# Performance work log

Measured on AMD Instinct MI355X. Metric: run time of the kernel, lower is better.

Reference implementation:

```python
import jax, jax.numpy as jnp
import numpy as np

EPS = 1e-12          # sinkhorn_knopp epsilon
LOW, HIGH = 0.02, 0.98  # SquashedSigmoid bounds
N_ITERS = 10         # num_iterations
BATCH = 2097152


def setup_inputs() -> dict:
    key = jax.random.key(0)
    ks = jax.random.split(key, 9)
    dims = [6, 64, 32, 16, 9]
    inp = {"margins": jax.random.uniform(ks[0], (BATCH, 6), jnp.float32, 0.05, 1.0)}
    for i in range(4):
        fi, fo = dims[i], dims[i + 1]
        inp[f"W{i+1}"] = jax.random.normal(ks[1 + 2 * i], (fi, fo), jnp.float32) / np.float32(np.sqrt(fi))
        inp[f"b{i+1}"] = jnp.zeros((fo,), jnp.float32)
    return inp


def _mlp(x, W1, b1, W2, b2, W3, b3, W4, b4):
    h = jax.nn.relu(x @ W1 + b1)
    h = jax.nn.relu(h @ W2 + b2)
    h = jax.nn.relu(h @ W3 + b3)
    return h @ W4 + b4  # [B, 9]


def _tau(p4):
    # user-supplied tau: 4 positive params -> 3x3 matrix; 2x2 block padded with ones
    B = p4.shape[0]
    A = jnp.ones((B, 3, 3), p4.dtype)
    return A.at[:, :2, :2].set(p4.reshape(B, 2, 2))


def _sinkhorn_knopp(A, r, c):
    # batched row/col balancing; per-sample A is 3x3, r/c are length-3 margins
    for _ in range(N_ITERS):
        A = A * (r[:, :, None] / (A.sum(axis=2, keepdims=True) + EPS))
        A = A * (c[:, None, :] / (A.sum(axis=1, keepdims=True) + EPS))
    return A


def reference(margins, W1, b1, W2, b2, W3, b3, W4, b4):
    B = margins.shape[0]
    M, F = margins[:, 0:3], margins[:, 3:6]
    pars = _mlp(margins, W1, b1, W2, b2, W3, b3, W4, b4)
    muc = _tau(jnp.exp(pars[:, 0:4]))                     # [B,3,3]
    sqs = lambda x: LOW + (HIGH - LOW) * jax.nn.sigmoid(x)
    shm, shf = sqs(pars[:, 4:6]), sqs(pars[:, 6:8])
    V = jnp.exp(pars[:, -1])                              # [B]
    ones = jnp.ones((B, 1), margins.dtype)
    shm0 = jnp.concatenate([shm, ones], axis=1)           # [B,3]
    shf0 = jnp.concatenate([shf, ones], axis=1)
    mucm0, muc0f = M * shm0, F * shf0                     # row / col margins
    mum0, mu0f = M * (1 - shm0), F * (1 - shf0)
    muc = _sinkhorn_knopp(muc, mucm0, muc0f)              # [B,3,3]
    top = jnp.concatenate([muc, mum0[:, :, None]], axis=2)                    # [B,3,4]
    bot = jnp.concatenate([mu0f[:, None, :], jnp.zeros((B, 1, 1), margins.dtype)], axis=2)  # [B,1,4]
    mus = jnp.concatenate([top, bot], axis=1)             # [B,4,4]
    return (mus, V)
```

## Files before the change

kernel.cpp:

```cpp
#include <hip/hip_runtime.h>

typedef _Float16 f16x8 __attribute__((ext_vector_type(8)));
typedef _Float16 f16x4 __attribute__((ext_vector_type(4)));
typedef __fp16   fp16x2 __attribute__((ext_vector_type(2)));
typedef float    f32x4 __attribute__((ext_vector_type(4)));

static constexpr float kLOW  = 0.02f;
static constexpr float kHIGH = 0.98f;

__device__ __forceinline__ float fast_rcp(float v) {
    return __builtin_amdgcn_rcpf(v);
}
__device__ __forceinline__ float fast_sigmoid(float v) {
    return fast_rcp(1.0f + __expf(-v));
}
__device__ __forceinline__ unsigned int relu_pk(float a, float b) {
    fp16x2 r = __builtin_amdgcn_cvt_pkrtz(fmaxf(a, 0.0f), fmaxf(b, 0.0f));
    return __builtin_bit_cast(unsigned int, r);
}

enum : int {
    WS_A1 = 0,
    WS_A2 = 4096,
    WS_A3 = 8192,
    WS_A4 = 9216,
    WS_B1 = 10240,
    WS_B2 = 14336,
    WS_B3 = 16384,
    WS_B4 = 17408,
    WS_TOTAL = 18432
};

__global__ __launch_bounds__(256) void prep_frags(
    const float* __restrict__ W1, const float* __restrict__ b1,
    const float* __restrict__ W2, const float* __restrict__ b2,
    const float* __restrict__ W3, const float* __restrict__ b3,
    const float* __restrict__ W4, const float* __restrict__ b4,
    char* __restrict__ ws)
{
    const int lane = threadIdx.x & 63;
    const int wid  = threadIdx.x >> 6;
    const int n16  = lane & 15;
    const int q    = lane >> 4;

    if (wid == 0) {
#pragma unroll
        for (int mt = 0; mt < 4; ++mt) {
            f16x8 a;
#pragma unroll
            for (int j = 0; j < 8; ++j) a[j] = (_Float16)0.0f;
            if (q == 0) {
#pragma unroll
                for (int j = 0; j < 6; ++j)
                    a[j] = (_Float16)W1[j * 64 + mt * 16 + n16];
            }
            ((f16x8*)(ws + WS_A1))[mt * 64 + lane] = a;
        }
#pragma unroll
        for (int mt = 0; mt < 4; ++mt)
            ((f32x4*)(ws + WS_B1))[mt * 64 + lane] = *(const f32x4*)(b1 + mt * 16 + q * 4);
    } else if (wid == 1) {
#pragma unroll
        for (int mt = 0; mt < 2; ++mt)
#pragma unroll
            for (int kt = 0; kt < 2; ++kt) {
                f16x8 a;
#pragma unroll
                for (int j = 0; j < 8; ++j)
                    a[j] = (_Float16)W2[(kt * 32 + q * 8 + j) * 32 + mt * 16 + n16];
                ((f16x8*)(ws + WS_A2))[(mt * 2 + kt) * 64 + lane] = a;
            }
    } else if (wid == 2) {
        f16x8 a3;
#pragma unroll
        for (int j = 0; j < 8; ++j)
            a3[j] = (_Float16)W3[(q * 8 + j) * 16 + n16];
        ((f16x8*)(ws + WS_A3))[lane] = a3;
        f16x8 a4;
#pragma unroll
        for (int j = 0; j < 8; ++j) {
            const int k = q * 8 + j;
            a4[j] = (k < 16 && n16 < 9) ? (_Float16)W4[k * 9 + n16] : (_Float16)0.0f;
        }
        ((f16x8*)(ws + WS_A4))[lane] = a4;
    } else {
#pragma unroll
        for (int mt = 0; mt < 2; ++mt)
            ((f32x4*)(ws + WS_B2))[mt * 64 + lane] = *(const f32x4*)(b2 + mt * 16 + q * 4);
        ((f32x4*)(ws + WS_B3))[lane] = *(const f32x4*)(b3 + q * 4);
        f32x4 bb;
#pragma unroll
        for (int r = 0; r < 4; ++r) {
            const int m = q * 4 + r;
            bb[r] = (m < 9) ? b4[m] : 0.0f;
        }
        ((f32x4*)(ws + WS_B4))[lane] = bb;
    }
}

__global__ __launch_bounds__(256, 4) void sinkhorn_mlp_mfma(
    const float* __restrict__ margins, const char* __restrict__ ws,
    float* __restrict__ out_mus, float* __restrict__ out_V, int B)
{
    __shared__ __align__(16) char smem_all[4 * 8192];
    const int lane = threadIdx.x & 63;
    const int wid  = threadIdx.x >> 6;
    char* smem = smem_all + wid * 8192;

    const int n16 = lane & 15;
    const int q   = lane >> 4;

    const int wbase = blockIdx.x * 256 + wid * 64;
    const int row   = wbase + lane;
    const int rowC  = row < B ? row : (B - 1);

    float x[6];
    {
        const float2* mp = (const float2*)(margins + (size_t)rowC * 6);
        const float2 a = mp[0], b = mp[1], c = mp[2];
        x[0] = a.x; x[1] = a.y; x[2] = b.x; x[3] = b.y; x[4] = c.x; x[5] = c.y;
    }

    {
        f16x8 xr;
#pragma unroll
        for (int j = 0; j < 8; ++j) xr[j] = (_Float16)0.0f;
#pragma unroll
        for (int i = 0; i < 6; ++i) xr[i] = (_Float16)x[i];
        *(f16x8*)(smem + 7168 + lane * 16) = xr;
    }

    f16x8 A1[4], A2w[2][2], A3w, A4w;
#pragma unroll
    for (int mt = 0; mt < 4; ++mt) A1[mt] = ((const f16x8*)(ws + WS_A1))[mt * 64 + lane];
#pragma unroll
    for (int mt = 0; mt < 2; ++mt)
#pragma unroll
        for (int kt = 0; kt < 2; ++kt)
            A2w[mt][kt] = ((const f16x8*)(ws + WS_A2))[(mt * 2 + kt) * 64 + lane];
    A3w = ((const f16x8*)(ws + WS_A3))[lane];
    A4w = ((const f16x8*)(ws + WS_A4))[lane];

    f32x4 b1v[4], b2v[2], b3v, b4v;
#pragma unroll
    for (int mt = 0; mt < 4; ++mt) b1v[mt] = ((const f32x4*)(ws + WS_B1))[mt * 64 + lane];
#pragma unroll
    for (int mt = 0; mt < 2; ++mt) b2v[mt] = ((const f32x4*)(ws + WS_B2))[mt * 64 + lane];
    b3v = ((const f32x4*)(ws + WS_B3))[lane];
    b4v = ((const f32x4*)(ws + WS_B4))[lane];

    f16x8 BX[4];
    if (q == 0) {
#pragma unroll
        for (int nt = 0; nt < 4; ++nt)
            BX[nt] = *(const f16x8*)(smem + 7168 + (nt * 16 + n16) * 16);
    } else {
#pragma unroll
        for (int nt = 0; nt < 4; ++nt)
#pragma unroll
            for (int j = 0; j < 8; ++j) BX[nt][j] = (_Float16)0.0f;
    }
#pragma unroll
    for (int mt = 0; mt < 4; ++mt) {
#pragma unroll
        for (int nt = 0; nt < 4; ++nt) {
            f32x4 C = b1v[mt];
            C = __builtin_amdgcn_mfma_f32_16x16x32_f16(A1[mt], BX[nt], C, 0, 0, 0);
            uint2 hv;
            hv.x = relu_pk(C[0], C[1]);
            hv.y = relu_pk(C[2], C[3]);
            const int r = nt * 16 + n16;
            const int col = (mt * 32 + q * 8) ^ ((r & 7) << 4);
            *(uint2*)(smem + r * 128 + col) = hv;
        }
    }

    f16x8 H1f[4][2];
#pragma unroll
    for (int nt = 0; nt < 4; ++nt) {
        const int r = nt * 16 + n16;
#pragma unroll
        for (int kt = 0; kt < 2; ++kt) {
            const int col = (kt * 64 + q * 16) ^ ((r & 7) << 4);
            H1f[nt][kt] = *(const f16x8*)(smem + r * 128 + col);
        }
    }
#pragma unroll
    for (int mt = 0; mt < 2; ++mt) {
#pragma unroll
        for (int nt = 0; nt < 4; ++nt) {
            f32x4 C = b2v[mt];
            C = __builtin_amdgcn_mfma_f32_16x16x32_f16(A2w[mt][0], H1f[nt][0], C, 0, 0, 0);
            C = __builtin_amdgcn_mfma_f32_16x16x32_f16(A2w[mt][1], H1f[nt][1], C, 0, 0, 0);
            uint2 hv;
            hv.x = relu_pk(C[0], C[1]);
            hv.y = relu_pk(C[2], C[3]);
            *(uint2*)(smem + (nt*16 + n16) * 80 + mt*32 + q*8) = hv;
        }
    }

    f16x8 H2f[4];
#pragma unroll
    for (int nt = 0; nt < 4; ++nt)
        H2f[nt] = *(const f16x8*)(smem + (nt*16 + n16) * 80 + q*16);
#pragma unroll
    for (int nt = 0; nt < 4; ++nt) {
        f32x4 C = b3v;
        C = __builtin_amdgcn_mfma_f32_16x16x32_f16(A3w, H2f[nt], C, 0, 0, 0);
        f16x4 hv;
#pragma unroll
        for (int r = 0; r < 4; ++r) hv[r] = (_Float16)fmaxf(C[r], 0.0f);
        *(f16x4*)(smem + (nt*16 + n16) * 32 + q*8) = hv;
    }

    f16x8 B4[4];
    if (q < 2) {
#pragma unroll
        for (int nt = 0; nt < 4; ++nt)
            B4[nt] = *(const f16x8*)(smem + (nt*16 + n16) * 32 + q * 16);
    } else {
#pragma unroll
        for (int nt = 0; nt < 4; ++nt)
#pragma unroll
            for (int j = 0; j < 8; ++j) B4[nt][j] = (_Float16)0.0f;
    }
#pragma unroll
    for (int nt = 0; nt < 4; ++nt) {
        f32x4 C = b4v;
        C = __builtin_amdgcn_mfma_f32_16x16x32_f16(A4w, B4[nt], C, 0, 0, 0);
        *(f32x4*)(smem + 2560 + (nt*16 + n16) * 80 + q * 16) = C;
    }

    float p[9];
    {
        const char* pr = smem + 2560 + lane * 80;
        *(f32x4*)&p[0] = *(const f32x4*)(pr);
        *(f32x4*)&p[4] = *(const f32x4*)(pr + 16);
        p[8] = *(const float*)(pr + 32);
    }

    const float K00 = __expf(p[0]), K01 = __expf(p[1]);
    const float K10 = __expf(p[2]), K11 = __expf(p[3]);

    const float sh_m0 = kLOW + (kHIGH - kLOW) * fast_sigmoid(p[4]);
    const float sh_m1 = kLOW + (kHIGH - kLOW) * fast_sigmoid(p[5]);
    const float sh_f0 = kLOW + (kHIGH - kLOW) * fast_sigmoid(p[6]);
    const float sh_f1 = kLOW + (kHIGH - kLOW) * fast_sigmoid(p[7]);
    const float V = __expf(p[8]);

    const float M0 = x[0], M1 = x[1], M2 = x[2];
    const float F0 = x[3], F1 = x[4], F2 = x[5];

    const float r0 = M0 * sh_m0, r1 = M1 * sh_m1, r2 = M2;
    const float c0 = F0 * sh_f0, c1 = F1 * sh_f1, c2 = F2;
    const float mum0_0 = M0 * (1.0f - sh_m0), mum0_1 = M1 * (1.0f - sh_m1);
    const float mu0f_0 = F0 * (1.0f - sh_f0), mu0f_1 = F1 * (1.0f - sh_f1);

    const float rc2 = fast_rcp(c2);
    const float g0 = c0 * rc2, g1 = c1 * rc2;
    float v0 = 1.0f, v1 = 1.0f;
    float u0, u1, u2;
#pragma unroll
    for (int it = 0; it < 9; ++it) {
        const float s0 = fmaf(K00, v0, fmaf(K01, v1, 1.0f));
        const float s1 = fmaf(K10, v0, fmaf(K11, v1, 1.0f));
        const float s2 = v0 + v1 + 1.0f;
        u0 = r0 * fast_rcp(s0);
        u1 = r1 * fast_rcp(s1);
        u2 = r2 * fast_rcp(s2);
        const float t0 = fmaf(K00, u0, fmaf(K10, u1, u2));
        const float t1 = fmaf(K01, u0, fmaf(K11, u1, u2));
        const float t2 = u0 + u1 + u2;
        v0 = g0 * (t2 * fast_rcp(t0));
        v1 = g1 * (t2 * fast_rcp(t1));
    }
    float vf0, vf1, vf2;
    {
        const float s0 = fmaf(K00, v0, fmaf(K01, v1, 1.0f));
        const float s1 = fmaf(K10, v0, fmaf(K11, v1, 1.0f));
        const float s2 = v0 + v1 + 1.0f;
        u0 = r0 * fast_rcp(s0);
        u1 = r1 * fast_rcp(s1);
        u2 = r2 * fast_rcp(s2);
        const float t0 = fmaf(K00, u0, fmaf(K10, u1, u2));
        const float t1 = fmaf(K01, u0, fmaf(K11, u1, u2));
        const float t2 = u0 + u1 + u2;
        vf0 = c0 * fast_rcp(t0);
        vf1 = c1 * fast_rcp(t1);
        vf2 = c2 * fast_rcp(t2);
    }
    const float A00 = u0 * K00 * vf0, A01 = u0 * K01 * vf1, A02 = u0 * vf2;
    const float A10 = u1 * K10 * vf0, A11 = u1 * K11 * vf1, A12 = u1 * vf2;
    const float A20 = u2 * vf0,       A21 = u2 * vf1,       A22 = u2 * vf2;

    {
        char* ob = smem + 2560;
        f32x4* s = (f32x4*)(ob + lane * 80);
        s[0] = f32x4{A00, A01, A02, mum0_0};
        s[1] = f32x4{A10, A11, A12, mum0_1};
        s[2] = f32x4{A20, A21, A22, 0.0f};
        s[3] = f32x4{mu0f_0, mu0f_1, 0.0f, 0.0f};

        if (wbase + 64 <= B) {
            float* og = out_mus + (size_t)wbase * 16;
#pragma unroll
            for (int k = 0; k < 4; ++k) {
                const int g = k * 64 + lane;
                const int r = g >> 2, c = g & 3;
                f32x4 v = *(const f32x4*)(ob + r * 80 + c * 16);
                *(f32x4*)(og + (size_t)g * 4) = v;
            }
            out_V[wbase + lane] = V;
        } else if (row < B) {
            float* og = out_mus + (size_t)row * 16;
            const char* sr = ob + lane * 80;
#pragma unroll
            for (int c = 0; c < 4; ++c)
                *(f32x4*)(og + c * 4) = *(const f32x4*)(sr + c * 16);
            out_V[row] = V;
        }
    }
}

extern "C" void kernel_launch(void* const* d_in, const int* in_sizes, int n_in,
                              void* d_out, int out_size, void* d_ws, size_t ws_size,
                              hipStream_t stream) {
    const float* margins = (const float*)d_in[0];
    const float* W1 = (const float*)d_in[1];
    const float* b1 = (const float*)d_in[2];
    const float* W2 = (const float*)d_in[3];
    const float* b2 = (const float*)d_in[4];
    const float* W3 = (const float*)d_in[5];
    const float* b3 = (const float*)d_in[6];
    const float* W4 = (const float*)d_in[7];
    const float* b4 = (const float*)d_in[8];

    const int B = in_sizes[0] / 6;
    float* out_mus = (float*)d_out;
    float* out_V   = out_mus + (size_t)B * 16;
    char*  ws      = (char*)d_ws;

    hipLaunchKernelGGL(prep_frags, dim3(1), dim3(256), 0, stream,
                       W1, b1, W2, b2, W3, b3, W4, b4, ws);

    dim3 block(256);
    dim3 grid((B + 255) / 256);
    hipLaunchKernelGGL(sinkhorn_mlp_mfma, grid, block, 0, stream,
                       margins, ws, out_mus, out_V, B);
}
```

Baseline: 214.1 us.

## Process two row groups per thread and pack Sinkhorn math into float2 vectors

Each wave now handles 128 rows in two halves, reusing the weight fragments loaded into registers, and the grid is halved. The Sinkhorn iteration and the elementwise math run on float2 pairs so the compiler can emit packed FP32 instructions and get more independent work per thread. W4 and b4 are pre-scaled by log2(e) so exp becomes a native exp2, removing a multiply per exponential. This raises register pressure, which may lower occupancy, and the store epilogue now runs twice per thread.

```diff
diff --git a/kernel.cpp b/kernel.cpp
--- a/kernel.cpp
+++ b/kernel.cpp
@@ -4,19 +4,40 @@
 typedef _Float16 f16x4 __attribute__((ext_vector_type(4)));
 typedef __fp16   fp16x2 __attribute__((ext_vector_type(2)));
 typedef float    f32x4 __attribute__((ext_vector_type(4)));
+typedef float    f32x2 __attribute__((ext_vector_type(2)));
 
 static constexpr float kLOW  = 0.02f;
 static constexpr float kHIGH = 0.98f;
+static constexpr float kLog2e = 1.44269504088896340736f;
 
 __device__ __forceinline__ float fast_rcp(float v) {
     return __builtin_amdgcn_rcpf(v);
 }
-__device__ __forceinline__ float fast_sigmoid(float v) {
-    return fast_rcp(1.0f + __expf(-v));
+__device__ __forceinline__ float fast_exp2(float v) {
+#if __has_builtin(__builtin_amdgcn_exp2f)
+    return __builtin_amdgcn_exp2f(v);
+#else
+    return exp2f(v);
+#endif
 }
 __device__ __forceinline__ unsigned int relu_pk(float a, float b) {
     fp16x2 r = __builtin_amdgcn_cvt_pkrtz(fmaxf(a, 0.0f), fmaxf(b, 0.0f));
     return __builtin_bit_cast(unsigned int, r);
+}
+
+__device__ __forceinline__ f32x2 fma2(f32x2 a, f32x2 b, f32x2 c) {
+    return f32x2{fmaf(a.x, b.x, c.x), fmaf(a.y, b.y, c.y)};
+}
+__device__ __forceinline__ f32x2 rcp2(f32x2 v) {
+    return f32x2{fast_rcp(v.x), fast_rcp(v.y)};
+}
+__device__ __forceinline__ f32x2 exp2_2(f32x2 v) {
+    return f32x2{fast_exp2(v.x), fast_exp2(v.y)};
+}
+__device__ __forceinline__ f32x2 sqs2(f32x2 v) {
+    f32x2 e = exp2_2(f32x2{-v.x, -v.y});
+    f32x2 s = rcp2(f32x2{1.0f + e.x, 1.0f + e.y});
+    return f32x2{kLOW + (kHIGH - kLOW) * s.x, kLOW + (kHIGH - kLOW) * s.y};
 }
 
 enum : int {
@@ -80,7 +101,8 @@
 #pragma unroll
         for (int j = 0; j < 8; ++j) {
             const int k = q * 8 + j;
-            a4[j] = (k < 16 && n16 < 9) ? (_Float16)W4[k * 9 + n16] : (_Float16)0.0f;
+            a4[j] = (k < 16 && n16 < 9) ? (_Float16)(W4[k * 9 + n16] * kLog2e)
+                                        : (_Float16)0.0f;
         }
         ((f16x8*)(ws + WS_A4))[lane] = a4;
     } else {
@@ -92,7 +114,7 @@
 #pragma unroll
         for (int r = 0; r < 4; ++r) {
             const int m = q * 4 + r;
-            bb[r] = (m < 9) ? b4[m] : 0.0f;
+            bb[r] = (m < 9) ? b4[m] * kLog2e : 0.0f;
         }
         ((f32x4*)(ws + WS_B4))[lane] = bb;
     }
@@ -110,24 +132,17 @@
     const int n16 = lane & 15;
     const int q   = lane >> 4;
 
-    const int wbase = blockIdx.x * 256 + wid * 64;
-    const int row   = wbase + lane;
-    const int rowC  = row < B ? row : (B - 1);
-
-    float x[6];
-    {
+    const int wbase = blockIdx.x * 512 + wid * 128;
+
+    float xx[2][6];
+#pragma unroll
+    for (int h = 0; h < 2; ++h) {
+        const int row  = wbase + h * 64 + lane;
+        const int rowC = row < B ? row : (B - 1);
         const float2* mp = (const float2*)(margins + (size_t)rowC * 6);
         const float2 a = mp[0], b = mp[1], c = mp[2];
-        x[0] = a.x; x[1] = a.y; x[2] = b.x; x[3] = b.y; x[4] = c.x; x[5] = c.y;
-    }
-
-    {
-        f16x8 xr;
-#pragma unroll
-        for (int j = 0; j < 8; ++j) xr[j] = (_Float16)0.0f;
-#pragma unroll
-        for (int i = 0; i < 6; ++i) xr[i] = (_Float16)x[i];
-        *(f16x8*)(smem + 7168 + lane * 16) = xr;
+        xx[h][0] = a.x; xx[h][1] = a.y; xx[h][2] = b.x;
+        xx[h][3] = b.y; xx[h][4] = c.x; xx[h][5] = c.y;
     }
 
     f16x8 A1[4], A2w[2][2], A3w, A4w;
@@ -149,160 +164,179 @@
     b3v = ((const f32x4*)(ws + WS_B3))[lane];
     b4v = ((const f32x4*)(ws + WS_B4))[lane];
 
-    f16x8 BX[4];
-    if (q == 0) {
+    float pp[2][9];
+#pragma unroll
+    for (int h = 0; h < 2; ++h) {
+        {
+            f16x8 xr;
+#pragma unroll
+            for (int j = 0; j < 8; ++j) xr[j] = (_Float16)0.0f;
+#pragma unroll
+            for (int i = 0; i < 6; ++i) xr[i] = (_Float16)xx[h][i];
+            *(f16x8*)(smem + 7168 + lane * 16) = xr;
+        }
+
+        f16x8 BX[4];
+        if (q == 0) {
+#pragma unroll
+            for (int nt = 0; nt < 4; ++nt)
+                BX[nt] = *(const f16x8*)(smem + 7168 + (nt * 16 + n16) * 16);
+        } else {
+#pragma unroll
+            for (int nt = 0; nt < 4; ++nt)
+#pragma unroll
+                for (int j = 0; j < 8; ++j) BX[nt][j] = (_Float16)0.0f;
+        }
+#pragma unroll
+        for (int mt = 0; mt < 4; ++mt) {
+#pragma unroll
+            for (int nt = 0; nt < 4; ++nt) {
+                f32x4 C = b1v[mt];
+                C = __builtin_amdgcn_mfma_f32_16x16x32_f16(A1[mt], BX[nt], C, 0, 0, 0);
+                uint2 hv;
+                hv.x = relu_pk(C[0], C[1]);
+                hv.y = relu_pk(C[2], C[3]);
+                const int r = nt * 16 + n16;
+                const int col = (mt * 32 + q * 8) ^ ((r & 7) << 4);
+                *(uint2*)(smem + r * 128 + col) = hv;
+            }
+        }
+
+        f16x8 H1f[4][2];
+#pragma unroll
+        for (int nt = 0; nt < 4; ++nt) {
+            const int r = nt * 16 + n16;
+#pragma unroll
+            for (int kt = 0; kt < 2; ++kt) {
+                const int col = (kt * 64 + q * 16) ^ ((r & 7) << 4);
+                H1f[nt][kt] = *(const f16x8*)(smem + r * 128 + col);
+            }
+        }
+#pragma unroll
+        for (int mt = 0; mt < 2; ++mt) {
+#pragma unroll
+            for (int nt = 0; nt < 4; ++nt) {
+                f32x4 C = b2v[mt];
+                C = __builtin_amdgcn_mfma_f32_16x16x32_f16(A2w[mt][0], H1f[nt][0], C, 0, 0, 0);
+                C = __builtin_amdgcn_mfma_f32_16x16x32_f16(A2w[mt][1], H1f[nt][1], C, 0, 0, 0);
+                uint2 hv;
+                hv.x = relu_pk(C[0], C[1]);
+                hv.y = relu_pk(C[2], C[3]);
+                *(uint2*)(smem + (nt*16 + n16) * 80 + mt*32 + q*8) = hv;
+            }
+        }
+
+        f16x8 H2f[4];
 #pragma unroll
         for (int nt = 0; nt < 4; ++nt)
-            BX[nt] = *(const f16x8*)(smem + 7168 + (nt * 16 + n16) * 16);
-    } else {
-#pragma unroll
-        for (int nt = 0; nt < 4; ++nt)
-#pragma unroll
-            for (int j = 0; j < 8; ++j) BX[nt][j] = (_Float16)0.0f;
-    }
-#pragma unroll
-    for (int mt = 0; mt < 4; ++mt) {
+            H2f[nt] = *(const f16x8*)(smem + (nt*16 + n16) * 80 + q*16);
 #pragma unroll
         for (int nt = 0; nt < 4; ++nt) {
-            f32x4 C = b1v[mt];
-            C = __builtin_amdgcn_mfma_f32_16x16x32_f16(A1[mt], BX[nt], C, 0, 0, 0);
-            uint2 hv;
-            hv.x = relu_pk(C[0], C[1]);
-            hv.y = relu_pk(C[2], C[3]);
-            const int r = nt * 16 + n16;
-            const int col = (mt * 32 + q * 8) ^ ((r & 7) << 4);
-            *(uint2*)(smem + r * 128 + col) = hv;
-        }
-    }
-
-    f16x8 H1f[4][2];
-#pragma unroll
-    for (int nt = 0; nt < 4; ++nt) {
-        const int r = nt * 16 + n16;
-#pragma unroll
-        for (int kt = 0; kt < 2; ++kt) {
-            const int col = (kt * 64 + q * 16) ^ ((r & 7) << 4);
-            H1f[nt][kt] = *(const f16x8*)(smem + r * 128 + col);
-        }
-    }
-#pragma unroll
-    for (int mt = 0; mt < 2; ++mt) {
+            f32x4 C = b3v;
+            C = __builtin_amdgcn_mfma_f32_16x16x32_f16(A3w, H2f[nt], C, 0, 0, 0);
+            f16x4 hv;
+#pragma unroll
+            for (int r = 0; r < 4; ++r) hv[r] = (_Float16)fmaxf(C[r], 0.0f);
+            *(f16x4*)(smem + (nt*16 + n16) * 32 + q*8) = hv;
+        }
+
+        f16x8 B4[4];
+        if (q < 2) {
+#pragma unroll
+            for (int nt = 0; nt < 4; ++nt)
+                B4[nt] = *(const f16x8*)(smem + (nt*16 + n16) * 32 + q * 16);
+        } else {
+#pragma unroll
+            for (int nt = 0; nt < 4; ++nt)
+#pragma unroll
+                for (int j = 0; j < 8; ++j) B4[nt][j] = (_Float16)0.0f;
+        }
 #pragma unroll
         for (int nt = 0; nt < 4; ++nt) {
-            f32x4 C = b2v[mt];
-            C = __builtin_amdgcn_mfma_f32_16x16x32_f16(A2w[mt][0], H1f[nt][0], C, 0, 0, 0);
-            C = __builtin_amdgcn_mfma_f32_16x16x32_f16(A2w[mt][1], H1f[nt][1], C, 0, 0, 0);
-            uint2 hv;
-            hv.x = relu_pk(C[0], C[1]);
-            hv.y = relu_pk(C[2], C[3]);
-            *(uint2*)(smem + (nt*16 + n16) * 80 + mt*32 + q*8) = hv;
-        }
-    }
-
-    f16x8 H2f[4];
-#pragma unroll
-    for (int nt = 0; nt < 4; ++nt)
-        H2f[nt] = *(const f16x8*)(smem + (nt*16 + n16) * 80 + q*16);
-#pragma unroll
-    for (int nt = 0; nt < 4; ++nt) {
-        f32x4 C = b3v;
-        C = __builtin_amdgcn_mfma_f32_16x16x32_f16(A3w, H2f[nt], C, 0, 0, 0);
-        f16x4 hv;
-#pragma unroll
-        for (int r = 0; r < 4; ++r) hv[r] = (_Float16)fmaxf(C[r], 0.0f);
-        *(f16x4*)(smem + (nt*16 + n16) * 32 + q*8) = hv;
-    }
-
-    f16x8 B4[4];
-    if (q < 2) {
-#pragma unroll
-        for (int nt = 0; nt < 4; ++nt)
-            B4[nt] = *(const f16x8*)(smem + (nt*16 + n16) * 32 + q * 16);
-    } else {
-#pragma unroll
-        for (int nt = 0; nt < 4; ++nt)
-#pragma unroll
-            for (int j = 0; j < 8; ++j) B4[nt][j] = (_Float16)0.0f;
-    }
-#pragma unroll
-    for (int nt = 0; nt < 4; ++nt) {
-        f32x4 C = b4v;
-        C = __builtin_amdgcn_mfma_f32_16x16x32_f16(A4w, B4[nt], C, 0, 0, 0);
-        *(f32x4*)(smem + 2560 + (nt*16 + n16) * 80 + q * 16) = C;
-    }
-
-    float p[9];
+            f32x4 C = b4v;
+            C = __builtin_amdgcn_mfma_f32_16x16x32_f16(A4w, B4[nt], C, 0, 0, 0);
+            *(f32x4*)(smem + 2560 + (nt*16 + n16) * 80 + q * 16) = C;
+        }
+
+        {
+            const char* pr = smem + 2560 + lane * 80;
+            f32x4 p0 = *(const f32x4*)(pr);
+            f32x4 p1 = *(const f32x4*)(pr + 16);
+#pragma unroll
+            for (int k = 0; k < 4; ++k) { pp[h][k] = p0[k]; pp[h][4+k] = p1[k]; }
+            pp[h][8] = *(const float*)(pr + 32);
+        }
+    }
+
+    f32x2 P[9];
+#pragma unroll
+    for (int k = 0; k < 9; ++k) P[k] = f32x2{pp[0][k], pp[1][k]};
+
+    const f32x2 K00 = exp2_2(P[0]), K01 = exp2_2(P[1]);
+    const f32x2 K10 = exp2_2(P[2]), K11 = exp2_2(P[3]);
+    const f32x2 sh_m0 = sqs2(P[4]), sh_m1 = sqs2(P[5]);
+    const f32x2 sh_f0 = sqs2(P[6]), sh_f1 = sqs2(P[7]);
+    const f32x2 Vv = exp2_2(P[8]);
+
+    const f32x2 M0 = {xx[0][0], xx[1][0]}, M1 = {xx[0][1], xx[1][1]}, M2 = {xx[0][2], xx[1][2]};
+    const f32x2 F0 = {xx[0][3], xx[1][3]}, F1 = {xx[0][4], xx[1][4]}, F2 = {xx[0][5], xx[1][5]};
+
+    const f32x2 one = {1.0f, 1.0f};
+    const f32x2 r0 = M0 * sh_m0, r1 = M1 * sh_m1, r2 = M2;
+    const f32x2 c0 = F0 * sh_f0, c1 = F1 * sh_f1, c2 = F2;
+    const f32x2 mum0_0 = M0 * (one - sh_m0), mum0_1 = M1 * (one - sh_m1);
+    const f32x2 mu0f_0 = F0 * (one - sh_f0), mu0f_1 = F1 * (one - sh_f1);
+
+    const f32x2 rc2 = rcp2(c2);
+    const f32x2 g0 = c0 * rc2, g1 = c1 * rc2;
+    f32x2 v0 = one, v1 = one;
+    f32x2 u0, u1, u2;
+#pragma unroll
+    for (int it = 0; it < 9; ++it) {
+        const f32x2 s0 = fma2(K00, v0, fma2(K01, v1, one));
+        const f32x2 s1 = fma2(K10, v0, fma2(K11, v1, one));
+        const f32x2 s2 = v0 + v1 + one;
+        u0 = r0 * rcp2(s0);
+        u1 = r1 * rcp2(s1);
+        u2 = r2 * rcp2(s2);
+        const f32x2 t0 = fma2(K00, u0, fma2(K10, u1, u2));
+        const f32x2 t1 = fma2(K01, u0, fma2(K11, u1, u2));
+        const f32x2 t2 = u0 + u1 + u2;
+        v0 = g0 * (t2 * rcp2(t0));
+        v1 = g1 * (t2 * rcp2(t1));
+    }
+    f32x2 vf0, vf1, vf2;
     {
-        const char* pr = smem + 2560 + lane * 80;
-        *(f32x4*)&p[0] = *(const f32x4*)(pr);
-        *(f32x4*)&p[4] = *(const f32x4*)(pr + 16);
-        p[8] = *(const float*)(pr + 32);
-    }
-
-    const float K00 = __expf(p[0]), K01 = __expf(p[1]);
-    const float K10 = __expf(p[2]), K11 = __expf(p[3]);
-
-    const float sh_m0 = kLOW + (kHIGH - kLOW) * fast_sigmoid(p[4]);
-    const float sh_m1 = kLOW + (kHIGH - kLOW) * fast_sigmoid(p[5]);
-    const float sh_f0 = kLOW + (kHIGH - kLOW) * fast_sigmoid(p[6]);
-    const float sh_f1 = kLOW + (kHIGH - kLOW) * fast_sigmoid(p[7]);
-    const float V = __expf(p[8]);
-
-    const float M0 = x[0], M1 = x[1], M2 = x[2];
-    const float F0 = x[3], F1 = x[4], F2 = x[5];
-
-    const float r0 = M0 * sh_m0, r1 = M1 * sh_m1, r2 = M2;
-    const float c0 = F0 * sh_f0, c1 = F1 * sh_f1, c2 = F2;
-    const float mum0_0 = M0 * (1.0f - sh_m0), mum0_1 = M1 * (1.0f - sh_m1);
-    const float mu0f_0 = F0 * (1.0f - sh_f0), mu0f_1 = F1 * (1.0f - sh_f1);
-
-    const float rc2 = fast_rcp(c2);
-    const float g0 = c0 * rc2, g1 = c1 * rc2;
-    float v0 = 1.0f, v1 = 1.0f;
-    float u0, u1, u2;
-#pragma unroll
-    for (int it = 0; it < 9; ++it) {
-        const float s0 = fmaf(K00, v0, fmaf(K01, v1, 1.0f));
-        const float s1 = fmaf(K10, v0, fmaf(K11, v1, 1.0f));
-        const float s2 = v0 + v1 + 1.0f;
-        u0 = r0 * fast_rcp(s0);
-        u1 = r1 * fast_rcp(s1);
-        u2 = r2 * fast_rcp(s2);
-        const float t0 = fmaf(K00, u0, fmaf(K10, u1, u2));
-        const float t1 = fmaf(K01, u0, fmaf(K11, u1, u2));
-        const float t2 = u0 + u1 + u2;
-        v0 = g0 * (t2 * fast_rcp(t0));
-        v1 = g1 * (t2 * fast_rcp(t1));
-    }
-    float vf0, vf1, vf2;
-    {
-        const float s0 = fmaf(K00, v0, fmaf(K01, v1, 1.0f));
-        const float s1 = fmaf(K10, v0, fmaf(K11, v1, 1.0f));
-        const float s2 = v0 + v1 + 1.0f;
-        u0 = r0 * fast_rcp(s0);
-        u1 = r1 * fast_rcp(s1);
-        u2 = r2 * fast_rcp(s2);
-        const float t0 = fmaf(K00, u0, fmaf(K10, u1, u2));
-        const float t1 = fmaf(K01, u0, fmaf(K11, u1, u2));
-        const float t2 = u0 + u1 + u2;
-        vf0 = c0 * fast_rcp(t0);
-        vf1 = c1 * fast_rcp(t1);
-        vf2 = c2 * fast_rcp(t2);
-    }
-    const float A00 = u0 * K00 * vf0, A01 = u0 * K01 * vf1, A02 = u0 * vf2;
-    const float A10 = u1 * K10 * vf0, A11 = u1 * K11 * vf1, A12 = u1 * vf2;
-    const float A20 = u2 * vf0,       A21 = u2 * vf1,       A22 = u2 * vf2;
-
-    {
+        const f32x2 s0 = fma2(K00, v0, fma2(K01, v1, one));
+        const f32x2 s1 = fma2(K10, v0, fma2(K11, v1, one));
+        const f32x2 s2 = v0 + v1 + one;
+        u0 = r0 * rcp2(s0);
+        u1 = r1 * rcp2(s1);
+        u2 = r2 * rcp2(s2);
+        const f32x2 t0 = fma2(K00, u0, fma2(K10, u1, u2));
+        const f32x2 t1 = fma2(K01, u0, fma2(K11, u1, u2));
+        const f32x2 t2 = u0 + u1 + u2;
+        vf0 = c0 * rcp2(t0);
+        vf1 = c1 * rcp2(t1);
+        vf2 = c2 * rcp2(t2);
+    }
+    const f32x2 A00 = u0 * K00 * vf0, A01 = u0 * K01 * vf1, A02 = u0 * vf2;
+    const f32x2 A10 = u1 * K10 * vf0, A11 = u1 * K11 * vf1, A12 = u1 * vf2;
+    const f32x2 A20 = u2 * vf0,       A21 = u2 * vf1,       A22 = u2 * vf2;
+
+#pragma unroll
+    for (int h = 0; h < 2; ++h) {
+        const int wb = wbase + h * 64;
+#define CO(v) (h == 0 ? (v).x : (v).y)
         char* ob = smem + 2560;
         f32x4* s = (f32x4*)(ob + lane * 80);
-        s[0] = f32x4{A00, A01, A02, mum0_0};
-        s[1] = f32x4{A10, A11, A12, mum0_1};
-        s[2] = f32x4{A20, A21, A22, 0.0f};
-        s[3] = f32x4{mu0f_0, mu0f_1, 0.0f, 0.0f};
-
-        if (wbase + 64 <= B) {
-            float* og = out_mus + (size_t)wbase * 16;
+        s[0] = f32x4{CO(A00), CO(A01), CO(A02), CO(mum0_0)};
+        s[1] = f32x4{CO(A10), CO(A11), CO(A12), CO(mum0_1)};
+        s[2] = f32x4{CO(A20), CO(A21), CO(A22), 0.0f};
+        s[3] = f32x4{CO(mu0f_0), CO(mu0f_1), 0.0f, 0.0f};
+
+        if (wb + 64 <= B) {
+            float* og = out_mus + (size_t)wb * 16;
 #pragma unroll
             for (int k = 0; k < 4; ++k) {
                 const int g = k * 64 + lane;
@@ -310,15 +344,16 @@
                 f32x4 v = *(const f32x4*)(ob + r * 80 + c * 16);
                 *(f32x4*)(og + (size_t)g * 4) = v;
             }
-            out_V[wbase + lane] = V;
-        } else if (row < B) {
-            float* og = out_mus + (size_t)row * 16;
+            out_V[wb + lane] = CO(Vv);
+        } else if (wb + lane < B) {
+            float* og = out_mus + (size_t)(wb + lane) * 16;
             const char* sr = ob + lane * 80;
 #pragma unroll
             for (int c = 0; c < 4; ++c)
                 *(f32x4*)(og + c * 4) = *(const f32x4*)(sr + c * 16);
-            out_V[row] = V;
-        }
+            out_V[wb + lane] = CO(Vv);
+        }
+#undef CO
     }
 }
 
@@ -344,7 +379,7 @@
                        W1, b1, W2, b2, W3, b3, W4, b4, ws);
 
     dim3 block(256);
-    dim3 grid((B + 255) / 256);
+    dim3 grid((B + 511) / 512);
     hipLaunchKernelGGL(sinkhorn_mlp_mfma, grid, block, 0, stream,
                        margins, ws, out_mus, out_V, B);
 }
```

Measured after the change: 270.1 us. 1.26x slower.
